# Kernel tuning notes

Hardware: AMD Instinct MI355X
Metric: run time of the kernel (lower is better)

The kernel has to match this reference:

```python
import jax, jax.numpy as jnp
import numpy as np

H1 = 768
H2 = 768
B, LQ, LK = 8, 1024, 1024


def setup_inputs() -> dict:
    key = jax.random.key(0)
    ks = jax.random.split(key, 12)
    s1 = 1.0 / np.sqrt(H1)
    s2 = 1.0 / np.sqrt(H2)
    # weights stored as [in, out] (equivalent to torch Linear weight.T)
    return {
        "tensor1": jax.random.normal(ks[0], (B, LQ, H1), jnp.float32),
        "tensor2": jax.random.normal(ks[1], (B, LK, H2), jnp.float32),
        "Wq": jax.random.uniform(ks[2], (3, H1, H2), jnp.float32, -s1, s1),
        "bq": jax.random.uniform(ks[3], (3, H2), jnp.float32, -s1, s1),
        "Wk": jax.random.uniform(ks[4], (3, H2, H2), jnp.float32, -s2, s2),
        "bk": jax.random.uniform(ks[5], (3, H2), jnp.float32, -s2, s2),
        "Wv": jax.random.uniform(ks[6], (3, H2, H2), jnp.float32, -s2, s2),
        "bv": jax.random.uniform(ks[7], (3, H2), jnp.float32, -s2, s2),
        "Wp": jax.random.uniform(ks[8], (3 * H2, H2), jnp.float32, -1.0 / np.sqrt(3 * H2), 1.0 / np.sqrt(3 * H2)),
        "bp": jax.random.uniform(ks[9], (H2,), jnp.float32, -1.0 / np.sqrt(3 * H2), 1.0 / np.sqrt(3 * H2)),
    }


def reference(tensor1, tensor2, Wq, bq, Wk, bk, Wv, bv, Wp, bp):
    # Three independent cross-attention heads, stacked on leading axis h=3.
    q = jnp.einsum("bqd,hde->hbqe", tensor1, Wq) + bq[:, None, None, :]  # [3,B,LQ,H2]
    k = jnp.einsum("bkd,hde->hbke", tensor2, Wk) + bk[:, None, None, :]  # [3,B,LK,H2]
    v = jnp.einsum("bkd,hde->hbke", tensor2, Wv) + bv[:, None, None, :]  # [3,B,LK,H2]
    scores = jnp.einsum("hbqe,hbke->hbqk", q, k)  # NOTE: no 1/sqrt(d) scaling, per original
    weights = jax.nn.softmax(scores, axis=-1)
    ctx = jnp.einsum("hbqk,hbke->hbqe", weights, v)  # [3,B,LQ,H2]
    # concat heads along feature dim -> [B,LQ,3*H2]
    multi = jnp.transpose(ctx, (1, 2, 0, 3)).reshape(ctx.shape[1], ctx.shape[2], -1)
    # project_multihead: ReLU then Linear
    return jax.nn.relu(multi) @ Wp + bp
```

## Files before the change

kernel.cpp:

```cpp
#include <hip/hip_runtime.h>
#include <hip/hip_bf16.h>


typedef _Float16 f16;
typedef __attribute__((ext_vector_type(8))) _Float16 f16x8;
typedef __attribute__((ext_vector_type(4))) float f32x4;
typedef __attribute__((ext_vector_type(4))) short s16x4;

#define DI __device__ __forceinline__

DI short f2hs(float f){
  f16 h = (f16)f;
  return __builtin_bit_cast(short, h);
}

DI f32x4 mfma16(f16x8 a, f16x8 b, f32x4 c){
  return __builtin_amdgcn_mfma_f32_16x16x32_f16(a, b, c, 0, 0, 0);
}

#define GLL16(gp, lp) __builtin_amdgcn_global_load_lds( \
    (const __attribute__((address_space(1))) unsigned int*)(gp), \
    (__attribute__((address_space(3))) unsigned int*)(lp), 16, 0, 0)

__global__ void cvt2_f16_kernel(const float* __restrict__ a, const float* __restrict__ b,
                                short* __restrict__ oa, short* __restrict__ ob, int n4each){
  int i = blockIdx.x * blockDim.x + threadIdx.x;
  const float* in = (i < n4each) ? a : b;
  short* out = (i < n4each) ? oa : ob;
  int j = (i < n4each) ? i : i - n4each;
  f32x4 v = ((const f32x4*)in)[j];
  s16x4 o;
  o[0]=f2hs(v[0]); o[1]=f2hs(v[1]); o[2]=f2hs(v[2]); o[3]=f2hs(v[3]);
  ((s16x4*)out)[j] = o;
}

__global__ void transpose_cvt_qkv_kernel(const float* __restrict__ Wq, const float* __restrict__ Wk,
                                         const float* __restrict__ Wv,
                                         short* __restrict__ WqT, short* __restrict__ WkT,
                                         short* __restrict__ WvT){
  __shared__ float tile[32][33];
  const int t = blockIdx.z / 3, hd = blockIdx.z % 3;
  const float* in = ((t==0)?Wq:(t==1)?Wk:Wv) + (long)hd*768*768;
  short* out = ((t==0)?WqT:(t==1)?WkT:WvT) + (long)hd*768*768;
  int c0 = blockIdx.x * 32, r0 = blockIdx.y * 32;
  int tx = threadIdx.x, ty = threadIdx.y;
  #pragma unroll
  for (int k=0;k<4;k++)
    tile[ty + k*8][tx] = in[(long)(r0 + ty + k*8) * 768 + c0 + tx];
  __syncthreads();
  #pragma unroll
  for (int k=0;k<4;k++)
    out[(long)(c0 + ty + k*8) * 768 + r0 + tx] = f2hs(tile[tx][ty + k*8]);
}

__global__ void transpose_cvt_kernel(const float* __restrict__ in, short* __restrict__ out, int R, int C){
  __shared__ float tile[32][33];
  int c0 = blockIdx.x * 32, r0 = blockIdx.y * 32;
  int tx = threadIdx.x, ty = threadIdx.y;
  #pragma unroll
  for (int k=0;k<4;k++)
    tile[ty + k*8][tx] = in[(long)(r0 + ty + k*8) * C + c0 + tx];
  __syncthreads();
  #pragma unroll
  for (int k=0;k<4;k++)
    out[(long)(c0 + ty + k*8) * R + r0 + tx] = f2hs(tile[tx][ty + k*8]);
}

DI void gemm_tile(const short* __restrict__ A, const short* __restrict__ Bt, int K,
                  int m0, int n0, short* As, short* Bs, f32x4 (&acc)[4][4])
{
  const int tid = threadIdx.x, wave = tid>>6, lane = tid&63;
  const int wm = wave>>1, wn = wave&1;
  const int fl = lane&15, fq = lane>>4;
  const int srow = lane>>2;
  const int scol = (((lane&3) ^ (srow&3)))*8;
  const int aswz = ((fq ^ (fl&3)))*8;
  for (int kk=0; kk<K; kk+=32){
    __syncthreads();
    #pragma unroll
    for (int r=0;r<2;r++){
      const int rb = r*64 + wave*16;
      GLL16(A  + (long)(m0+rb+srow)*K + kk + scol, As + rb*32);
      GLL16(Bt + (long)(n0+rb+srow)*K + kk + scol, Bs + rb*32);
    }
    __syncthreads();
    f16x8 a[4];
    #pragma unroll
    for (int i=0;i<4;i++) a[i] = *(const f16x8*)(As + (wm*64+i*16+fl)*32 + aswz);
    #pragma unroll
    for (int j=0;j<4;j++){
      f16x8 b = *(const f16x8*)(Bs + (wn*64+j*16+fl)*32 + aswz);
      #pragma unroll
      for (int i=0;i<4;i++) acc[i][j] = mfma16(a[i], b, acc[i][j]);
    }
  }
}

__global__ __launch_bounds__(256,2) void gemm_qkv_kernel(
    const short* __restrict__ t1b, const short* __restrict__ t2b,
    const short* __restrict__ WqT, const short* __restrict__ WkT, const short* __restrict__ WvT,
    const float* __restrict__ bq, const float* __restrict__ bk, const float* __restrict__ bv,
    short* __restrict__ Qb, short* __restrict__ Kb, short* __restrict__ Vtb)
{
  __shared__ short As[128*32];
  __shared__ short Bs[128*32];
  const int z = blockIdx.z;
  const int h = z % 3, which = z / 3;
  const short* A  = (which==0) ? t1b : t2b;
  const short* Bt = ((which==0)?WqT:(which==1)?WkT:WvT) + h*768*768;
  const float* bias = ((which==0)?bq:(which==1)?bk:bv) + h*768;
  const int m0 = blockIdx.x*128, n0 = blockIdx.y*128;
  const int tid = threadIdx.x, wave = tid>>6, lane = tid&63;
  const int wm = wave>>1, wn = wave&1;
  const int fl = lane&15, fq = lane>>4;

  f32x4 vz = {0.f,0.f,0.f,0.f};
  f32x4 acc[4][4];
  #pragma unroll
  for (int i=0;i<4;i++)
    #pragma unroll
    for (int j=0;j<4;j++) acc[i][j] = vz;

  gemm_tile(A, Bt, 768, m0, n0, As, Bs, acc);

  if (which < 2){
    short* outp = (which==0 ? Qb : Kb) + (long)h*8192*768;
    #pragma unroll
    for (int j=0;j<4;j++){
      int col = n0 + wn*64 + j*16 + fl;
      float bb = bias[col];
      #pragma unroll
      for (int i=0;i<4;i++){
        int row = m0 + wm*64 + i*16 + fq*4;
        #pragma unroll
        for (int r=0;r<4;r++)
          outp[(long)(row+r)*768 + col] = f2hs(acc[i][j][r] + bb);
      }
    }
  } else {
    const int bidx = m0 >> 10;
    const int lk0  = m0 & 1023;
    short* outp = Vtb + (long)(h*8 + bidx)*768*1024;
    #pragma unroll
    for (int j=0;j<4;j++){
      int e = n0 + wn*64 + j*16 + fl;
      float bb = bias[e];
      #pragma unroll
      for (int i=0;i<4;i++){
        int lk = lk0 + wm*64 + i*16 + fq*4;
        s16x4 pack;
        #pragma unroll
        for (int r=0;r<4;r++) pack[r] = f2hs(acc[i][j][r] + bb);
        *(s16x4*)(outp + (long)e*1024 + lk) = pack;
      }
    }
  }
}

__global__ __launch_bounds__(256,2) void qk_exp_kernel(
    const short* __restrict__ Qb, const short* __restrict__ Kb,
    short* __restrict__ P, float* __restrict__ Mx, float* __restrict__ Lx)
{
  __shared__ short As[128*32];
  __shared__ short Bs[128*32];
  __shared__ float red0[2][2][64];
  __shared__ float red1[2][2][64];
  const int qt = blockIdx.x, ct = blockIdx.y, hb = blockIdx.z;
  const int h = hb >> 3, b = hb & 7;
  const int tid = threadIdx.x, wave = tid>>6, lane = tid&63;
  const int wm = wave>>1, wn = wave&1;
  const int fl = lane&15, fq = lane>>4;
  const short* Abase = Qb + ((long)h*8192 + b*1024)*768;
  const short* Bbase = Kb + ((long)h*8192 + b*1024)*768;

  f32x4 vz = {0.f,0.f,0.f,0.f};
  f32x4 acc[4][4];
  #pragma unroll
  for (int i=0;i<4;i++)
    #pragma unroll
    for (int j=0;j<4;j++) acc[i][j] = vz;

  gemm_tile(Abase, Bbase, 768, qt*128, ct*128, As, Bs, acc);

  float mt[4][4];
  #pragma unroll
  for (int i=0;i<4;i++)
    #pragma unroll
    for (int r=0;r<4;r++){
      float m = acc[i][0][r];
      #pragma unroll
      for (int j=1;j<4;j++) m = fmaxf(m, acc[i][j][r]);
      m = fmaxf(m, __shfl_xor(m, 1));
      m = fmaxf(m, __shfl_xor(m, 2));
      m = fmaxf(m, __shfl_xor(m, 4));
      m = fmaxf(m, __shfl_xor(m, 8));
      mt[i][r] = m;
      if (fl == 0) red0[wn][wm][i*16 + fq*4 + r] = m;
    }
  __syncthreads();
  #pragma unroll
  for (int i=0;i<4;i++)
    #pragma unroll
    for (int r=0;r<4;r++)
      mt[i][r] = fmaxf(red0[0][wm][i*16 + fq*4 + r], red0[1][wm][i*16 + fq*4 + r]);

  #pragma unroll
  for (int i=0;i<4;i++)
    #pragma unroll
    for (int r=0;r<4;r++){
      float s = 0.f;
      #pragma unroll
      for (int j=0;j<4;j++){
        float p = __expf(acc[i][j][r] - mt[i][r]);
        acc[i][j][r] = p;
        s += p;
      }
      s += __shfl_xor(s, 1);
      s += __shfl_xor(s, 2);
      s += __shfl_xor(s, 4);
      s += __shfl_xor(s, 8);
      if (fl == 0) red1[wn][wm][i*16 + fq*4 + r] = s;
    }
  __syncthreads();

  #pragma unroll
  for (int j=0;j<4;j++){
    int c = ct*128 + wn*64 + j*16 + fl;
    #pragma unroll
    for (int i=0;i<4;i++){
      int q = qt*128 + wm*64 + i*16 + fq*4;
      #pragma unroll
      for (int r=0;r<4;r++)
        P[((long)hb*1024 + q + r)*1024 + c] = f2hs(acc[i][j][r]);
    }
  }
  if (fl == 0 && wn == 0){
    long aux = ((long)(hb*8 + ct))*1024 + qt*128;
    #pragma unroll
    for (int i=0;i<4;i++)
      #pragma unroll
      for (int r=0;r<4;r++){
        int row = wm*64 + i*16 + fq*4 + r;
        Mx[aux + row] = mt[i][r];
        Lx[aux + row] = red1[0][wm][row & 63] + red1[1][wm][row & 63];
      }
  }
}

__global__ void softmax_factor_kernel(const float* __restrict__ Mx, const float* __restrict__ Lx,
                                      short* __restrict__ Sc){
  int idx = blockIdx.x * 256 + threadIdx.x;
  int hb = idx >> 10, q = idx & 1023;
  float m[8], l[8];
  #pragma unroll
  for (int t=0;t<8;t++){
    long a = ((long)(hb*8 + t))*1024 + q;
    m[t] = Mx[a];
    l[t] = Lx[a];
  }
  float mg = m[0];
  #pragma unroll
  for (int t=1;t<8;t++) mg = fmaxf(mg, m[t]);
  float lg = 0.f;
  #pragma unroll
  for (int t=0;t<8;t++) lg += l[t] * __expf(m[t] - mg);
  float inv = 1.0f / lg;
  #pragma unroll
  for (int t=0;t<8;t++)
    Sc[((long)(hb*8 + t))*1024 + q] = f2hs(__expf(m[t] - mg) * inv);
}

__global__ __launch_bounds__(256,2) void pv_kernel(
    const short* __restrict__ P, const short* __restrict__ Vtb,
    const short* __restrict__ Sc, short* __restrict__ multi)
{
  __shared__ short As[128*32];
  __shared__ short Bs[128*32];
  const int qt = blockIdx.x, et = blockIdx.y, hb = blockIdx.z;
  const int h = hb >> 3, b = hb & 7;
  const int tid = threadIdx.x, wave = tid>>6, lane = tid&63;
  const int wm = wave>>1, wn = wave&1;
  const int fl = lane&15, fq = lane>>4;
  const int srow = lane>>2;
  const int scol = (((lane&3) ^ (srow&3)))*8;
  const int aswz = ((fq ^ (fl&3)))*8;
  const short* Abase = P + (long)hb*1024*1024 + (long)(qt*128)*1024;
  const short* Bbase = Vtb + (long)hb*768*1024 + (long)(et*128)*1024;
  const short* scp = Sc + (long)(hb*8)*1024 + qt*128;

  f32x4 vz = {0.f,0.f,0.f,0.f};
  f32x4 acc[4][4];
  #pragma unroll
  for (int i=0;i<4;i++)
    #pragma unroll
    for (int j=0;j<4;j++) acc[i][j] = vz;

  for (int ct=0; ct<8; ct++){
    f16 s[4];
    #pragma unroll
    for (int i=0;i<4;i++)
      s[i] = __builtin_bit_cast(f16, scp[ct*1024 + wm*64 + i*16 + fl]);
    #pragma unroll
    for (int t=0;t<4;t++){
      const int kk = ct*128 + t*32;
      __syncthreads();
      #pragma unroll
      for (int r=0;r<2;r++){
        const int rb = r*64 + wave*16;
        GLL16(Abase + (long)(rb+srow)*1024 + kk + scol, As + rb*32);
        GLL16(Bbase + (long)(rb+srow)*1024 + kk + scol, Bs + rb*32);
      }
      __syncthreads();
      f16x8 a[4];
      #pragma unroll
      for (int i=0;i<4;i++){
        f16x8 av = *(const f16x8*)(As + (wm*64+i*16+fl)*32 + aswz);
        f16x8 sv;
        #pragma unroll
        for (int e=0;e<8;e++) sv[e] = s[i];
        a[i] = av * sv;
      }
      #pragma unroll
      for (int j=0;j<4;j++){
        f16x8 bv = *(const f16x8*)(Bs + (wn*64+j*16+fl)*32 + aswz);
        #pragma unroll
        for (int i=0;i<4;i++) acc[i][j] = mfma16(a[i], bv, acc[i][j]);
      }
    }
  }

  short* mp = multi + (long)(b*1024 + qt*128)*2304 + h*768 + et*128;
  #pragma unroll
  for (int j=0;j<4;j++){
    int e = wn*64 + j*16 + fl;
    #pragma unroll
    for (int i=0;i<4;i++){
      int q = wm*64 + i*16 + fq*4;
      #pragma unroll
      for (int r=0;r<4;r++)
        mp[(long)(q+r)*2304 + e] = f2hs(fmaxf(acc[i][j][r], 0.f));
    }
  }
}

__global__ __launch_bounds__(256,2) void gemm_out_kernel(
    const short* __restrict__ A, const short* __restrict__ Bt,
    const float* __restrict__ bias, float* __restrict__ out)
{
  __shared__ short As[128*32];
  __shared__ short Bs[128*32];
  const int m0 = blockIdx.x*128, n0 = blockIdx.y*128;
  const int tid = threadIdx.x, wave = tid>>6, lane = tid&63;
  const int wm = wave>>1, wn = wave&1;
  const int fl = lane&15, fq = lane>>4;

  f32x4 vz = {0.f,0.f,0.f,0.f};
  f32x4 acc[4][4];
  #pragma unroll
  for (int i=0;i<4;i++)
    #pragma unroll
    for (int j=0;j<4;j++) acc[i][j] = vz;

  gemm_tile(A, Bt, 2304, m0, n0, As, Bs, acc);

  #pragma unroll
  for (int j=0;j<4;j++){
    int col = n0 + wn*64 + j*16 + fl;
    float bb = bias[col];
    #pragma unroll
    for (int i=0;i<4;i++){
      int row = m0 + wm*64 + i*16 + fq*4;
      #pragma unroll
      for (int r=0;r<4;r++)
        out[(long)(row+r)*768 + col] = acc[i][j][r] + bb;
    }
  }
}

extern "C" void kernel_launch(void* const* d_in, const int* in_sizes, int n_in,
                              void* d_out, int out_size, void* d_ws, size_t ws_size,
                              hipStream_t stream)
{
  const float* t1 = (const float*)d_in[0];
  const float* t2 = (const float*)d_in[1];
  const float* Wq = (const float*)d_in[2];
  const float* bq = (const float*)d_in[3];
  const float* Wk = (const float*)d_in[4];
  const float* bk = (const float*)d_in[5];
  const float* Wv = (const float*)d_in[6];
  const float* bv = (const float*)d_in[7];
  const float* Wp = (const float*)d_in[8];
  const float* bp = (const float*)d_in[9];
  float* out = (float*)d_out;

  char* ws = (char*)d_ws;
  size_t off = 0;
  auto carve = [&](size_t bytes){ void* p = ws + off; off += (bytes + 255) & ~(size_t)255; return p; };
  short* t1b = (short*)carve(8L*1024*768*2);
  short* t2b = (short*)carve(8L*1024*768*2);
  short* WqT = (short*)carve(3L*768*768*2);
  short* WkT = (short*)carve(3L*768*768*2);
  short* WvT = (short*)carve(3L*768*768*2);
  short* WpT = (short*)carve(768L*2304*2);
  short* Qb  = (short*)carve(3L*8192*768*2);
  short* Kb  = (short*)carve(3L*8192*768*2);
  short* Vtb = (short*)carve(3L*8*768*1024*2);
  short* Pb  = (short*)carve(24L*1024*1024*2);
  float* Mx  = (float*)carve(24L*8*1024*4);
  float* Lx  = (float*)carve(24L*8*1024*4);
  short* Scb = (short*)carve(24L*8*1024*2);
  short* multib = Qb;

  cvt2_f16_kernel<<<12288, 256, 0, stream>>>(t1, t2, t1b, t2b, 1572864);
  transpose_cvt_qkv_kernel<<<dim3(24,24,9), dim3(32,8), 0, stream>>>(Wq, Wk, Wv, WqT, WkT, WvT);
  transpose_cvt_kernel<<<dim3(24,72,1), dim3(32,8), 0, stream>>>(Wp, WpT, 2304, 768);
  gemm_qkv_kernel<<<dim3(64,6,9), 256, 0, stream>>>(t1b,t2b,WqT,WkT,WvT,bq,bk,bv,Qb,Kb,Vtb);
  qk_exp_kernel<<<dim3(8,8,24), 256, 0, stream>>>(Qb, Kb, Pb, Mx, Lx);
  softmax_factor_kernel<<<96, 256, 0, stream>>>(Mx, Lx, Scb);
  pv_kernel<<<dim3(8,6,24), 256, 0, stream>>>(Pb, Vtb, Scb, multib);
  gemm_out_kernel<<<dim3(64,6,1), 256, 0, stream>>>(multib, WpT, bp, out);
}
```

Baseline: 443.8 us.

## Fold Wk into Wq to eliminate K projection, use column bias for scores

```diff
diff --git a/kernel.cpp b/kernel.cpp
--- a/kernel.cpp
+++ b/kernel.cpp
@@ -6,12 +6,16 @@
 typedef __attribute__((ext_vector_type(8))) _Float16 f16x8;
 typedef __attribute__((ext_vector_type(4))) float f32x4;
 typedef __attribute__((ext_vector_type(4))) short s16x4;
+typedef __attribute__((ext_vector_type(8))) short s16x8;
 
 #define DI __device__ __forceinline__
 
 DI short f2hs(float f){
   f16 h = (f16)f;
   return __builtin_bit_cast(short, h);
+}
+DI float hs2f(short s){
+  return (float)__builtin_bit_cast(f16, s);
 }
 
 DI f32x4 mfma16(f16x8 a, f16x8 b, f32x4 c){
@@ -34,27 +38,10 @@
   ((s16x4*)out)[j] = o;
 }
 
-__global__ void transpose_cvt_qkv_kernel(const float* __restrict__ Wq, const float* __restrict__ Wk,
-                                         const float* __restrict__ Wv,
-                                         short* __restrict__ WqT, short* __restrict__ WkT,
-                                         short* __restrict__ WvT){
-  __shared__ float tile[32][33];
-  const int t = blockIdx.z / 3, hd = blockIdx.z % 3;
-  const float* in = ((t==0)?Wq:(t==1)?Wk:Wv) + (long)hd*768*768;
-  short* out = ((t==0)?WqT:(t==1)?WkT:WvT) + (long)hd*768*768;
-  int c0 = blockIdx.x * 32, r0 = blockIdx.y * 32;
-  int tx = threadIdx.x, ty = threadIdx.y;
-  #pragma unroll
-  for (int k=0;k<4;k++)
-    tile[ty + k*8][tx] = in[(long)(r0 + ty + k*8) * 768 + c0 + tx];
-  __syncthreads();
-  #pragma unroll
-  for (int k=0;k<4;k++)
-    out[(long)(c0 + ty + k*8) * 768 + r0 + tx] = f2hs(tile[tx][ty + k*8]);
-}
-
 __global__ void transpose_cvt_kernel(const float* __restrict__ in, short* __restrict__ out, int R, int C){
   __shared__ float tile[32][33];
+  long zoff = (long)blockIdx.z * R * C;
+  in += zoff; out += zoff;
   int c0 = blockIdx.x * 32, r0 = blockIdx.y * 32;
   int tx = threadIdx.x, ty = threadIdx.y;
   #pragma unroll
@@ -96,19 +83,87 @@
   }
 }
 
-__global__ __launch_bounds__(256,2) void gemm_qkv_kernel(
+__global__ __launch_bounds__(256,2) void gemm_m_kernel(
+    const short* __restrict__ WqH, const short* __restrict__ WkH, short* __restrict__ Mt)
+{
+  __shared__ short As[128*32];
+  __shared__ short Bs[128*32];
+  const int h = blockIdx.z;
+  const int m0 = blockIdx.x*128, n0 = blockIdx.y*128;
+  const int tid = threadIdx.x, wave = tid>>6, lane = tid&63;
+  const int wm = wave>>1, wn = wave&1;
+  const int fl = lane&15, fq = lane>>4;
+
+  f32x4 vz = {0.f,0.f,0.f,0.f};
+  f32x4 acc[4][4];
+  #pragma unroll
+  for (int i=0;i<4;i++)
+    #pragma unroll
+    for (int j=0;j<4;j++) acc[i][j] = vz;
+
+  gemm_tile(WqH + (long)h*768*768, WkH + (long)h*768*768, 768, m0, n0, As, Bs, acc);
+
+  short* outp = Mt + (long)h*768*768;
+  #pragma unroll
+  for (int j=0;j<4;j++){
+    int col = n0 + wn*64 + j*16 + fl;
+    #pragma unroll
+    for (int i=0;i<4;i++){
+      int row = m0 + wm*64 + i*16 + fq*4;
+      s16x4 pack;
+      #pragma unroll
+      for (int r=0;r<4;r++) pack[r] = f2hs(acc[i][j][r]);
+      *(s16x4*)(outp + (long)col*768 + row) = pack;
+    }
+  }
+}
+
+__global__ void vvec_kernel(const short* __restrict__ WkH, const float* __restrict__ bq,
+                            float* __restrict__ v){
+  __shared__ float bql[768];
+  const int h = blockIdx.x;
+  for (int i=threadIdx.x;i<768;i+=256) bql[i] = bq[h*768+i];
+  __syncthreads();
+  for (int d=threadIdx.x; d<768; d+=256){
+    const s16x8* row = (const s16x8*)(WkH + ((long)h*768 + d)*768);
+    float s = 0.f;
+    for (int c=0;c<96;c++){
+      s16x8 w = row[c];
+      #pragma unroll
+      for (int e=0;e<8;e++) s += hs2f(w[e]) * bql[c*8+e];
+    }
+    v[h*768+d] = s;
+  }
+}
+
+__global__ void colbias_kernel(const short* __restrict__ t2b, const float* __restrict__ v,
+                               float* __restrict__ vb){
+  __shared__ float vl[768];
+  const int hb = blockIdx.x, h = hb>>3, b = hb&7;
+  for (int i=threadIdx.x;i<768;i+=256) vl[i] = v[h*768+i];
+  __syncthreads();
+  const int r = blockIdx.y*256 + threadIdx.x;
+  const s16x8* row = (const s16x8*)(t2b + ((long)b*1024 + r)*768);
+  float s = 0.f;
+  for (int c=0;c<96;c++){
+    s16x8 w = row[c];
+    #pragma unroll
+    for (int e=0;e<8;e++) s += hs2f(w[e]) * vl[c*8+e];
+  }
+  vb[(long)hb*1024 + r] = s;
+}
+
+__global__ __launch_bounds__(256,2) void gemm_gv_kernel(
     const short* __restrict__ t1b, const short* __restrict__ t2b,
-    const short* __restrict__ WqT, const short* __restrict__ WkT, const short* __restrict__ WvT,
-    const float* __restrict__ bq, const float* __restrict__ bk, const float* __restrict__ bv,
-    short* __restrict__ Qb, short* __restrict__ Kb, short* __restrict__ Vtb)
+    const short* __restrict__ Mt, const short* __restrict__ WvT,
+    const float* __restrict__ bv, short* __restrict__ Gb, short* __restrict__ Vtb)
 {
   __shared__ short As[128*32];
   __shared__ short Bs[128*32];
   const int z = blockIdx.z;
   const int h = z % 3, which = z / 3;
   const short* A  = (which==0) ? t1b : t2b;
-  const short* Bt = ((which==0)?WqT:(which==1)?WkT:WvT) + h*768*768;
-  const float* bias = ((which==0)?bq:(which==1)?bk:bv) + h*768;
+  const short* Bt = ((which==0)?Mt:WvT) + (long)h*768*768;
   const int m0 = blockIdx.x*128, n0 = blockIdx.y*128;
   const int tid = threadIdx.x, wave = tid>>6, lane = tid&63;
   const int wm = wave>>1, wn = wave&1;
@@ -123,21 +178,21 @@
 
   gemm_tile(A, Bt, 768, m0, n0, As, Bs, acc);
 
-  if (which < 2){
-    short* outp = (which==0 ? Qb : Kb) + (long)h*8192*768;
+  if (which == 0){
+    short* outp = Gb + (long)h*8192*768;
     #pragma unroll
     for (int j=0;j<4;j++){
       int col = n0 + wn*64 + j*16 + fl;
-      float bb = bias[col];
       #pragma unroll
       for (int i=0;i<4;i++){
         int row = m0 + wm*64 + i*16 + fq*4;
         #pragma unroll
         for (int r=0;r<4;r++)
-          outp[(long)(row+r)*768 + col] = f2hs(acc[i][j][r] + bb);
+          outp[(long)(row+r)*768 + col] = f2hs(acc[i][j][r]);
       }
     }
   } else {
+    const float* bias = bv + h*768;
     const int bidx = m0 >> 10;
     const int lk0  = m0 & 1023;
     short* outp = Vtb + (long)(h*8 + bidx)*768*1024;
@@ -158,7 +213,7 @@
 }
 
 __global__ __launch_bounds__(256,2) void qk_exp_kernel(
-    const short* __restrict__ Qb, const short* __restrict__ Kb,
+    const short* __restrict__ Gb, const short* __restrict__ t2b, const float* __restrict__ vb,
     short* __restrict__ P, float* __restrict__ Mx, float* __restrict__ Lx)
 {
   __shared__ short As[128*32];
@@ -170,8 +225,8 @@
   const int tid = threadIdx.x, wave = tid>>6, lane = tid&63;
   const int wm = wave>>1, wn = wave&1;
   const int fl = lane&15, fq = lane>>4;
-  const short* Abase = Qb + ((long)h*8192 + b*1024)*768;
-  const short* Bbase = Kb + ((long)h*8192 + b*1024)*768;
+  const short* Abase = Gb + ((long)h*8192 + b*1024)*768;
+  const short* Bbase = t2b + (long)b*1024*768;
 
   f32x4 vz = {0.f,0.f,0.f,0.f};
   f32x4 acc[4][4];
@@ -181,6 +236,17 @@
     for (int j=0;j<4;j++) acc[i][j] = vz;
 
   gemm_tile(Abase, Bbase, 768, qt*128, ct*128, As, Bs, acc);
+
+  const float* vbp = vb + (long)hb*1024 + ct*128;
+  float cb[4];
+  #pragma unroll
+  for (int j=0;j<4;j++) cb[j] = vbp[wn*64 + j*16 + fl];
+  #pragma unroll
+  for (int i=0;i<4;i++)
+    #pragma unroll
+    for (int j=0;j<4;j++)
+      #pragma unroll
+      for (int r=0;r<4;r++) acc[i][j][r] += cb[j];
 
   float mt[4][4];
   #pragma unroll
@@ -322,9 +388,9 @@
       }
       #pragma unroll
       for (int j=0;j<4;j++){
-        f16x8 bv = *(const f16x8*)(Bs + (wn*64+j*16+fl)*32 + aswz);
+        f16x8 bvv = *(const f16x8*)(Bs + (wn*64+j*16+fl)*32 + aswz);
         #pragma unroll
-        for (int i=0;i<4;i++) acc[i][j] = mfma16(a[i], bv, acc[i][j]);
+        for (int i=0;i<4;i++) acc[i][j] = mfma16(a[i], bvv, acc[i][j]);
       }
     }
   }
@@ -386,7 +452,6 @@
   const float* Wq = (const float*)d_in[2];
   const float* bq = (const float*)d_in[3];
   const float* Wk = (const float*)d_in[4];
-  const float* bk = (const float*)d_in[5];
   const float* Wv = (const float*)d_in[6];
   const float* bv = (const float*)d_in[7];
   const float* Wp = (const float*)d_in[8];
@@ -398,24 +463,30 @@
   auto carve = [&](size_t bytes){ void* p = ws + off; off += (bytes + 255) & ~(size_t)255; return p; };
   short* t1b = (short*)carve(8L*1024*768*2);
   short* t2b = (short*)carve(8L*1024*768*2);
-  short* WqT = (short*)carve(3L*768*768*2);
-  short* WkT = (short*)carve(3L*768*768*2);
+  short* WqH = (short*)carve(3L*768*768*2);
+  short* WkH = (short*)carve(3L*768*768*2);
   short* WvT = (short*)carve(3L*768*768*2);
   short* WpT = (short*)carve(768L*2304*2);
-  short* Qb  = (short*)carve(3L*8192*768*2);
-  short* Kb  = (short*)carve(3L*8192*768*2);
+  short* Mt  = (short*)carve(3L*768*768*2);
+  short* Gb  = (short*)carve(3L*8192*768*2);
   short* Vtb = (short*)carve(3L*8*768*1024*2);
   short* Pb  = (short*)carve(24L*1024*1024*2);
   float* Mx  = (float*)carve(24L*8*1024*4);
   float* Lx  = (float*)carve(24L*8*1024*4);
   short* Scb = (short*)carve(24L*8*1024*2);
-  short* multib = Qb;
+  float* vvb = (float*)carve(3L*768*4);
+  float* vb  = (float*)carve(24L*1024*4);
+  short* multib = Gb;
 
   cvt2_f16_kernel<<<12288, 256, 0, stream>>>(t1, t2, t1b, t2b, 1572864);
-  transpose_cvt_qkv_kernel<<<dim3(24,24,9), dim3(32,8), 0, stream>>>(Wq, Wk, Wv, WqT, WkT, WvT);
+  cvt2_f16_kernel<<<3456, 256, 0, stream>>>(Wq, Wk, WqH, WkH, 442368);
+  transpose_cvt_kernel<<<dim3(24,24,3), dim3(32,8), 0, stream>>>(Wv, WvT, 768, 768);
   transpose_cvt_kernel<<<dim3(24,72,1), dim3(32,8), 0, stream>>>(Wp, WpT, 2304, 768);
-  gemm_qkv_kernel<<<dim3(64,6,9), 256, 0, stream>>>(t1b,t2b,WqT,WkT,WvT,bq,bk,bv,Qb,Kb,Vtb);
-  qk_exp_kernel<<<dim3(8,8,24), 256, 0, stream>>>(Qb, Kb, Pb, Mx, Lx);
+  gemm_m_kernel<<<dim3(6,6,3), 256, 0, stream>>>(WqH, WkH, Mt);
+  vvec_kernel<<<3, 256, 0, stream>>>(WkH, bq, vvb);
+  colbias_kernel<<<dim3(24,4), 256, 0, stream>>>(t2b, vvb, vb);
+  gemm_gv_kernel<<<dim3(64,6,6), 256, 0, stream>>>(t1b, t2b, Mt, WvT, bv, Gb, Vtb);
+  qk_exp_kernel<<<dim3(8,8,24), 256, 0, stream>>>(Gb, t2b, vb, Pb, Mx, Lx);
   softmax_factor_kernel<<<96, 256, 0, stream>>>(Mx, Lx, Scb);
   pv_kernel<<<dim3(8,6,24), 256, 0, stream>>>(Pb, Vtb, Scb, multib);
   gemm_out_kernel<<<dim3(64,6,1), 256, 0, stream>>>(multib, WpT, bp, out);
```

Result: slower. 478.3 us (+7.8%).
